# Kernel optimization log

Hardware: AMD Instinct MI355X
Metric: run time of the kernel (lower is better)

Reference implementation:

```python
import jax, jax.numpy as jnp
import numpy as np

N = 100000      # nodes
E = 800000      # edges (avg degree 8)
D_IN = 128      # in_channels
HEADS = 8
C = 16          # out_channels per head (heads*C = 128 output dim)
NEG_SLOPE = 0.2  # PyG GATConv default leaky_relu slope


def setup_inputs() -> dict:
    key = jax.random.key(0)
    ks = jax.random.split(key, 12)
    s = 1.0 / np.sqrt(D_IN)
    x = jax.random.normal(ks[0], (N, D_IN), jnp.float32)
    ei = jax.random.randint(ks[1], (2, E), 0, N, jnp.int32)
    return {
        "x": x,
        "ei": ei,
        # conv_in GATConv params
        "W_in": jax.random.normal(ks[2], (D_IN, HEADS * C), jnp.float32) * s,
        "a_src_in": jax.random.normal(ks[3], (HEADS, C), jnp.float32) * s,
        "a_dst_in": jax.random.normal(ks[4], (HEADS, C), jnp.float32) * s,
        "b_in": jnp.zeros((HEADS * C,), jnp.float32),
        # conv_out GATConv params (applied to flipped edges)
        "W_out": jax.random.normal(ks[5], (D_IN, HEADS * C), jnp.float32) * s,
        "a_src_out": jax.random.normal(ks[6], (HEADS, C), jnp.float32) * s,
        "a_dst_out": jax.random.normal(ks[7], (HEADS, C), jnp.float32) * s,
        "b_out": jnp.zeros((HEADS * C,), jnp.float32),
    }


def _gat_conv(x, src, dst, W, a_src, a_dst, b):
    # h: [N, H, C] projected node features
    h = (x @ W).reshape(N, HEADS, C)
    # per-node attention logits [N, H]
    alpha_src = jnp.einsum("nhc,hc->nh", h, a_src)
    alpha_dst = jnp.einsum("nhc,hc->nh", h, a_dst)
    # per-edge logits, message flows src -> dst; softmax grouped by dst
    logits = jax.nn.leaky_relu(alpha_src[src] + alpha_dst[dst], NEG_SLOPE)  # [E, H]
    seg_max = jax.ops.segment_max(logits, dst, num_segments=N)              # [N, H]
    ex = jnp.exp(logits - seg_max[dst])
    denom = jax.ops.segment_sum(ex, dst, num_segments=N)                    # [N, H]
    coef = ex / denom[dst]                                                  # [E, H]
    msg = h[src] * coef[:, :, None]                                         # [E, H, C]
    out = jax.ops.segment_sum(msg, dst, num_segments=N)                     # [N, H, C]
    return out.reshape(N, HEADS * C) + b


def reference(x, ei, W_in, a_src_in, a_dst_in, b_in, W_out, a_src_out, a_dst_out, b_out):
    src, dst = ei[0], ei[1]
    # DirSeq: conv_in on (src->dst), conv_out on flipped edges (dst->src)
    x_in = _gat_conv(x, src, dst, W_in, a_src_in, a_dst_in, b_in)
    x_out = _gat_conv(x, dst, src, W_out, a_src_out, a_dst_out, b_out)
    return x_in + x_out
```

## Files before the change

### kernel.cpp

```cpp
#include <hip/hip_runtime.h>

#define N_NODES 100000
#define N_EDGES 800000
#define NEG 0.2f
#define PB_SHIFT 8
#define PB_NODES 256
#define N_PBKT ((N_NODES + PB_NODES - 1) / PB_NODES)
#define TILE_E 4096
#define EPT 16
#define PREP_BLOCKS ((N_NODES * 128 / 4 + 255) / 256)
#define HIST_BLOCKS 192

typedef __attribute__((ext_vector_type(8))) short bf16x8;
typedef __attribute__((ext_vector_type(4))) float f32x4;

__device__ inline unsigned short f2bf(float f) {
    unsigned u = __float_as_uint(f);
    u += 0x7fffu + ((u >> 16) & 1u);
    return (unsigned short)(u >> 16);
}
__device__ inline float bf2f_lo(unsigned u) { return __uint_as_float(u << 16); }
__device__ inline float bf2f_hi(unsigned u) { return __uint_as_float(u & 0xffff0000u); }

__global__ __launch_bounds__(256) void prep_w_kernel(
    const float* __restrict__ W_in, const float* __restrict__ W_out,
    const float* __restrict__ as_in, const float* __restrict__ ad_in,
    const float* __restrict__ as_out, const float* __restrict__ ad_out,
    unsigned short* __restrict__ Wf, int* __restrict__ bcnt)
{
    const int t = blockIdx.x * 256 + threadIdx.x;
    if (t < 2 * N_PBKT) bcnt[t] = 0;
    if (t >= 2 * 4 * 9 * 64) return;
    const int lane = t & 63;
    const int rest = t >> 6;
    const int ct  = rest % 9;
    const int kb  = (rest / 9) & 3;
    const int dir = rest / 36;
    const float* W  = dir ? W_out  : W_in;
    const float* as = dir ? as_out : as_in;
    const float* ad = dir ? ad_out : ad_in;
    const int m16 = lane & 15, quad = lane >> 4;

    bf16x8 o;
#pragma unroll
    for (int j = 0; j < 8; ++j) {
        const int k = kb * 32 + quad * 8 + j;
        float v;
        if (ct < 8) {
            v = W[k * 128 + ct * 16 + m16];
        } else {
            const float* av = (m16 < 8) ? as : ad;
            const int hh = m16 & 7;
            v = 0.f;
            for (int c = 0; c < 16; ++c)
                v += W[k * 128 + hh * 16 + c] * av[hh * 16 + c];
        }
        o[j] = (short)f2bf(v);
    }
    *(bf16x8*)&Wf[(long long)t * 8] = o;
}

__global__ __launch_bounds__(256) void prep_hist_kernel(
    const float* __restrict__ x, unsigned short* __restrict__ x_bf,
    const int* __restrict__ ei, int* __restrict__ bcnt)
{
    const int tid = threadIdx.x;
    if (blockIdx.x < PREP_BLOCKS) {
        const int i = (blockIdx.x * 256 + tid) * 4;
        if (i >= N_NODES * 128) return;
        const float4 v = *(const float4*)&x[i];
        ushort4 o;
        o.x = f2bf(v.x); o.y = f2bf(v.y); o.z = f2bf(v.z); o.w = f2bf(v.w);
        *(ushort4*)&x_bf[i] = o;
        return;
    }
    __shared__ int bh[2 * N_PBKT];
    for (int i = tid; i < 2 * N_PBKT; i += 256) bh[i] = 0;
    __syncthreads();
    const int hb = blockIdx.x - PREP_BLOCKS;
    for (int e = hb * 256 + tid; e < N_EDGES; e += HIST_BLOCKS * 256) {
        const int s = ei[e];
        const int t = ei[N_EDGES + e];
        atomicAdd(&bh[t >> PB_SHIFT], 1);
        atomicAdd(&bh[N_PBKT + (s >> PB_SHIFT)], 1);
    }
    __syncthreads();
    for (int i = tid; i < 2 * N_PBKT; i += 256) {
        const int v = bh[i];
        if (v) atomicAdd(&bcnt[i], v);
    }
}

__global__ __launch_bounds__(256) void gemm_kernel(
    const unsigned short* __restrict__ x_bf,
    const unsigned short* __restrict__ Wf,
    unsigned short* __restrict__ h_in, unsigned short* __restrict__ h_out,
    float* __restrict__ asrc_in, float* __restrict__ adst_in,
    float* __restrict__ asrc_out, float* __restrict__ adst_out)
{
    const int dir = blockIdx.y;
    unsigned short* h = dir ? h_out : h_in;
    float* asrc = dir ? asrc_out : asrc_in;
    float* adst = dir ? adst_out : adst_in;

    const int tid  = threadIdx.x;
    const int lane = tid & 63;
    const int wave = tid >> 6;
    const int m16  = lane & 15;
    const int quad = lane >> 4;
    const int rbase = blockIdx.x * 128 + wave * 32;

    f32x4 acc[2][8];
    f32x4 acc_a[2];
#pragma unroll
    for (int rt = 0; rt < 2; ++rt) {
        acc_a[rt] = f32x4{0.f, 0.f, 0.f, 0.f};
#pragma unroll
        for (int ct = 0; ct < 8; ++ct)
            acc[rt][ct] = f32x4{0.f, 0.f, 0.f, 0.f};
    }

    const unsigned short* wf = Wf + (long long)dir * 4 * 9 * 64 * 8;

#pragma unroll
    for (int kb = 0; kb < 4; ++kb) {
        const int k0 = kb * 32 + quad * 8;
        bf16x8 a[2];
#pragma unroll
        for (int rt = 0; rt < 2; ++rt) {
            int r = rbase + rt * 16 + m16;
            r = r < N_NODES ? r : N_NODES - 1;
            a[rt] = *(const bf16x8*)&x_bf[(long long)r * 128 + k0];
        }
#pragma unroll
        for (int ct = 0; ct < 9; ++ct) {
            const bf16x8 b = *(const bf16x8*)&wf[(long long)((kb * 9 + ct) * 64 + lane) * 8];
            if (ct < 8) {
                acc[0][ct] = __builtin_amdgcn_mfma_f32_16x16x32_bf16(a[0], b, acc[0][ct], 0, 0, 0);
                acc[1][ct] = __builtin_amdgcn_mfma_f32_16x16x32_bf16(a[1], b, acc[1][ct], 0, 0, 0);
            } else {
                acc_a[0] = __builtin_amdgcn_mfma_f32_16x16x32_bf16(a[0], b, acc_a[0], 0, 0, 0);
                acc_a[1] = __builtin_amdgcn_mfma_f32_16x16x32_bf16(a[1], b, acc_a[1], 0, 0, 0);
            }
        }
    }

#pragma unroll
    for (int rt = 0; rt < 2; ++rt) {
#pragma unroll
        for (int r = 0; r < 4; ++r) {
            const int row = rbase + rt * 16 + quad * 4 + r;
            if (row < N_NODES) {
                unsigned short* hp = &h[(long long)row * 128 + m16];
#pragma unroll
                for (int ct = 0; ct < 8; ++ct)
                    hp[ct * 16] = f2bf(acc[rt][ct][r]);
                const float av = acc_a[rt][r];
                if (m16 < 8) asrc[row * 8 + m16] = av;
                else         adst[row * 8 + (m16 - 8)] = av;
            }
        }
    }
}

__global__ __launch_bounds__(512) void bucket_scan_kernel(
    const int* __restrict__ bcnt,
    int* __restrict__ boffs0, int* __restrict__ boffs1,
    int* __restrict__ gcur,
    int* __restrict__ offs_in, int* __restrict__ offs_out)
{
    const int dir = blockIdx.x;
    const int* c = bcnt + dir * N_PBKT;
    int* bo = dir ? boffs1 : boffs0;
    int* gc = gcur + dir * N_PBKT;

    __shared__ int sm[512];
    const int tid = threadIdx.x;
    const int v = (tid < N_PBKT) ? c[tid] : 0;
    sm[tid] = v;
    __syncthreads();
#pragma unroll
    for (int off = 1; off < 512; off <<= 1) {
        int t = (tid >= off) ? sm[tid - off] : 0;
        __syncthreads();
        sm[tid] += t;
        __syncthreads();
    }
    if (tid < N_PBKT) {
        const int excl = sm[tid] - v;
        bo[tid] = excl;
        gc[tid] = excl;
    }
    if (tid == N_PBKT - 1) bo[N_PBKT] = sm[tid];
    if (tid == 0) (dir ? offs_out : offs_in)[N_NODES] = N_EDGES;
}

__global__ __launch_bounds__(256) void partition_kernel(
    const int* __restrict__ ei, int* __restrict__ gcur,
    int* __restrict__ binned0, int* __restrict__ binned1)
{
    const int dir = blockIdx.y;
    int* binned = dir ? binned1 : binned0;
    int* gc = gcur + dir * N_PBKT;

    __shared__ int hist[N_PBKT];
    __shared__ int curs[N_PBKT];
    const int tid = threadIdx.x;
    for (int i = tid; i < N_PBKT; i += 256) hist[i] = 0;
    __syncthreads();

    const int e0 = blockIdx.x * TILE_E;
    int key[EPT], val[EPT];
#pragma unroll
    for (int i = 0; i < EPT; ++i) {
        const int e = e0 + i * 256 + tid;
        if (e < N_EDGES) {
            const int s = ei[e];
            const int t = ei[N_EDGES + e];
            key[i] = dir ? s : t;
            val[i] = dir ? t : s;
            atomicAdd(&hist[key[i] >> PB_SHIFT], 1);
        } else {
            key[i] = -1; val[i] = 0;
        }
    }
    __syncthreads();
    for (int b = tid; b < N_PBKT; b += 256) {
        const int c = hist[b];
        curs[b] = c ? atomicAdd(&gc[b], c) : 0;
    }
    __syncthreads();
#pragma unroll
    for (int i = 0; i < EPT; ++i) {
        if (key[i] >= 0) {
            const int pos = atomicAdd(&curs[key[i] >> PB_SHIFT], 1);
            binned[pos] = (val[i] << 8) | (key[i] & (PB_NODES - 1));
        }
    }
}

__global__ __launch_bounds__(256) void place_kernel(
    const int* __restrict__ binned0, const int* __restrict__ binned1,
    const int* __restrict__ boffs0, const int* __restrict__ boffs1,
    int* __restrict__ adj_in, int* __restrict__ adj_out,
    int* __restrict__ offs_in, int* __restrict__ offs_out)
{
    const int b   = blockIdx.x;
    const int dir = blockIdx.y;
    const int* bp = dir ? binned1 : binned0;
    const int* bo = dir ? boffs1  : boffs0;
    int* adj  = dir ? adj_out  : adj_in;
    int* offs = dir ? offs_out : offs_in;

    const int base = b << PB_SHIFT;
    const int beg = bo[b], end = bo[b + 1];
    const int tid = threadIdx.x;

    __shared__ int cnt[PB_NODES];
    __shared__ int sc[PB_NODES];
    __shared__ int cur[PB_NODES];

    cnt[tid] = 0;
    __syncthreads();
    for (int p = beg + tid; p < end; p += 256)
        atomicAdd(&cnt[bp[p] & (PB_NODES - 1)], 1);
    __syncthreads();
    const int v = cnt[tid];
    sc[tid] = v;
    __syncthreads();
#pragma unroll
    for (int off = 1; off < PB_NODES; off <<= 1) {
        int t = (tid >= off) ? sc[tid - off] : 0;
        __syncthreads();
        sc[tid] += t;
        __syncthreads();
    }
    const int excl = beg + sc[tid] - v;
    cur[tid] = excl;
    const int node = base + tid;
    if (node < N_NODES) offs[node] = excl;
    __syncthreads();
    for (int p = beg + tid; p < end; p += 256) {
        const int pk = bp[p];
        adj[atomicAdd(&cur[pk & (PB_NODES - 1)], 1)] = pk >> 8;
    }
}

__global__ __launch_bounds__(256) void gather_kernel(
    const int* __restrict__ offs_in, const int* __restrict__ adj_in,
    const int* __restrict__ offs_out, const int* __restrict__ adj_out,
    const unsigned short* __restrict__ h_in, const unsigned short* __restrict__ h_out,
    const float* __restrict__ asrc_in, const float* __restrict__ adst_in,
    const float* __restrict__ asrc_out, const float* __restrict__ adst_out,
    const float* __restrict__ b_in, const float* __restrict__ b_out,
    float* __restrict__ out)
{
    const int n = (blockIdx.x * 256 + threadIdx.x) >> 6;
    if (n >= N_NODES) return;
    const int lane = threadIdx.x & 63;
    const int c0 = lane * 2;
    const int hh = lane >> 3;
    const int g8 = lane & 7;
    const int grpbase = lane & 56;

    float acc0 = b_in[c0] + b_out[c0];
    float acc1 = b_in[c0 + 1] + b_out[c0 + 1];

#define DIR_BLOCK(OFFS, ADJ, HX, ASRC, ADST)                                   \
    {                                                                          \
        const int beg = OFFS[n], end = OFFS[n + 1];                            \
        if (end > beg) {                                                       \
            const float ad = ADST[n * 8 + hh];                                 \
            float num0 = 0.f, num1 = 0.f, den = 0.f;                           \
            int p = beg;                                                       \
            for (; p + 8 <= end; p += 8) {                                     \
                const int nb_mine = ADJ[p + g8];                               \
                float l = ASRC[nb_mine * 8 + hh] + ad;                         \
                l = l > 0.f ? l : NEG * l;                                     \
                const float w = __expf(l);                                     \
                den += w;                                                      \
                _Pragma("unroll")                                              \
                for (int g = 0; g < 8; ++g) {                                  \
                    const int   nb_g = __shfl(nb_mine, grpbase + g, 64);       \
                    const float w_g  = __shfl(w, grpbase + g, 64);             \
                    const unsigned hv = *(const unsigned*)&HX[(long long)nb_g * 128 + c0]; \
                    num0 += w_g * bf2f_lo(hv);                                 \
                    num1 += w_g * bf2f_hi(hv);                                 \
                }                                                              \
            }                                                                  \
            if (p < end) {                                                     \
                const int q = p + g8;                                          \
                const int nb_mine = (q < end) ? ADJ[q] : 0;                    \
                float w = 0.f;                                                 \
                if (q < end) {                                                 \
                    float l = ASRC[nb_mine * 8 + hh] + ad;                     \
                    l = l > 0.f ? l : NEG * l;                                 \
                    w = __expf(l);                                             \
                }                                                              \
                den += w;                                                      \
                const int cnt_t = end - p;                                     \
                for (int g = 0; g < cnt_t; ++g) {                              \
                    const int   nb_g = __shfl(nb_mine, grpbase + g, 64);       \
                    const float w_g  = __shfl(w, grpbase + g, 64);             \
                    const unsigned hv = *(const unsigned*)&HX[(long long)nb_g * 128 + c0]; \
                    num0 += w_g * bf2f_lo(hv);                                 \
                    num1 += w_g * bf2f_hi(hv);                                 \
                }                                                              \
            }                                                                  \
            den += __shfl_xor(den, 1, 64);                                     \
            den += __shfl_xor(den, 2, 64);                                     \
            den += __shfl_xor(den, 4, 64);                                     \
            acc0 += num0 / den;                                                \
            acc1 += num1 / den;                                                \
        }                                                                      \
    }

    DIR_BLOCK(offs_in, adj_in, h_in, asrc_in, adst_in)
    DIR_BLOCK(offs_out, adj_out, h_out, asrc_out, adst_out)
#undef DIR_BLOCK

    *(float2*)&out[(long long)n * 128 + c0] = float2{acc0, acc1};
}

extern "C" void kernel_launch(void* const* d_in, const int* in_sizes, int n_in,
                              void* d_out, int out_size, void* d_ws, size_t ws_size,
                              hipStream_t stream) {
    const float* x      = (const float*)d_in[0];
    const int*   ei     = (const int*)  d_in[1];
    const float* W_in   = (const float*)d_in[2];
    const float* as_in  = (const float*)d_in[3];
    const float* ad_in  = (const float*)d_in[4];
    const float* b_in   = (const float*)d_in[5];
    const float* W_out  = (const float*)d_in[6];
    const float* as_out = (const float*)d_in[7];
    const float* ad_out = (const float*)d_in[8];
    const float* b_out  = (const float*)d_in[9];
    float* out = (float*)d_out;

    char* ws = (char*)d_ws;
    const long long NH = (long long)N_NODES * 128;
    unsigned short* x_bf  = (unsigned short*)ws;    ws += NH * 2;
    unsigned short* h_in  = (unsigned short*)ws;    ws += NH * 2;
    unsigned short* h_out = (unsigned short*)ws;    ws += NH * 2;
    unsigned short* Wf    = (unsigned short*)ws;    ws += 2LL * 4 * 9 * 64 * 8 * 2;
    float* asrc_in   = (float*)ws;                  ws += N_NODES * 8 * 4;
    float* adst_in   = (float*)ws;                  ws += N_NODES * 8 * 4;
    float* asrc_out  = (float*)ws;                  ws += N_NODES * 8 * 4;
    float* adst_out  = (float*)ws;                  ws += N_NODES * 8 * 4;
    int* binned0     = (int*)ws;                    ws += (long long)N_EDGES * 4;
    int* binned1     = (int*)ws;                    ws += (long long)N_EDGES * 4;
    int* adj_in      = (int*)ws;                    ws += N_EDGES * 4;
    int* adj_out     = (int*)ws;                    ws += N_EDGES * 4;
    int* offs_in     = (int*)ws;                    ws += (N_NODES + 1) * 4;
    int* offs_out    = (int*)ws;                    ws += (N_NODES + 1) * 4;
    int* bcnt        = (int*)ws;                    ws += 2 * N_PBKT * 4;
    int* boffs0      = (int*)ws;                    ws += (N_PBKT + 1) * 4;
    int* boffs1      = (int*)ws;                    ws += (N_PBKT + 1) * 4;
    int* gcur        = (int*)ws;                    ws += 2 * N_PBKT * 4;

    prep_w_kernel<<<(2 * 4 * 9 * 64 + 255) / 256, 256, 0, stream>>>(
        W_in, W_out, as_in, ad_in, as_out, ad_out, Wf, bcnt);
    prep_hist_kernel<<<PREP_BLOCKS + HIST_BLOCKS, 256, 0, stream>>>(
        x, x_bf, ei, bcnt);

    dim3 gemm_grid((N_NODES + 127) / 128, 2);
    gemm_kernel<<<gemm_grid, 256, 0, stream>>>(
        x_bf, Wf, h_in, h_out, asrc_in, adst_in, asrc_out, adst_out);

    bucket_scan_kernel<<<2, 512, 0, stream>>>(
        bcnt, boffs0, boffs1, gcur, offs_in, offs_out);
    partition_kernel<<<dim3((N_EDGES + TILE_E - 1) / TILE_E, 2), 256, 0, stream>>>(
        ei, gcur, binned0, binned1);
    place_kernel<<<dim3(N_PBKT, 2), 256, 0, stream>>>(
        binned0, binned1, boffs0, boffs1, adj_in, adj_out, offs_in, offs_out);

    gather_kernel<<<(N_NODES * 64 + 255) / 256, 256, 0, stream>>>(
        offs_in, adj_in, offs_out, adj_out, h_in, h_out,
        asrc_in, adst_in, asrc_out, adst_out, b_in, b_out, out);
}
```

Baseline: 302.8 us.

## Precompute per-edge attention weights in place kernel, simplify gather loop

Moves the per-edge leaky-relu and exp computation from the gather kernel into the CSR placement kernel, which writes an edge-ordered [E,8] weight array alongside adj. The gather then reads precomputed weights and uniform (scalar) adjacency loads in a single loop with tail masking, using readfirstlane on the node index and a reciprocal instead of two divides. This removes random asrc gathers and exp work from the gather's critical path. In exchange it adds about 51 MB of extra weight writes and reads, plus padding writes for the masked tail.

```diff
diff --git a/kernel.cpp b/kernel.cpp
--- a/kernel.cpp
+++ b/kernel.cpp
@@ -21,15 +21,23 @@
 }
 __device__ inline float bf2f_lo(unsigned u) { return __uint_as_float(u << 16); }
 __device__ inline float bf2f_hi(unsigned u) { return __uint_as_float(u & 0xffff0000u); }
+__device__ inline float lexp(float l) { return __expf(l > 0.f ? l : NEG * l); }
 
 __global__ __launch_bounds__(256) void prep_w_kernel(
     const float* __restrict__ W_in, const float* __restrict__ W_out,
     const float* __restrict__ as_in, const float* __restrict__ ad_in,
     const float* __restrict__ as_out, const float* __restrict__ ad_out,
-    unsigned short* __restrict__ Wf, int* __restrict__ bcnt)
+    unsigned short* __restrict__ Wf, int* __restrict__ bcnt,
+    int* __restrict__ adj_in, int* __restrict__ adj_out,
+    float* __restrict__ w_in, float* __restrict__ w_out)
 {
     const int t = blockIdx.x * 256 + threadIdx.x;
     if (t < 2 * N_PBKT) bcnt[t] = 0;
+    if (t < 8) { adj_in[N_EDGES + t] = 0; adj_out[N_EDGES + t] = 0; }
+    if (t < 64) {
+        w_in[(long long)N_EDGES * 8 + t] = 0.f;
+        w_out[(long long)N_EDGES * 8 + t] = 0.f;
+    }
     if (t >= 2 * 4 * 9 * 64) return;
     const int lane = t & 63;
     const int rest = t >> 6;
@@ -243,7 +251,10 @@
     const int* __restrict__ binned0, const int* __restrict__ binned1,
     const int* __restrict__ boffs0, const int* __restrict__ boffs1,
     int* __restrict__ adj_in, int* __restrict__ adj_out,
-    int* __restrict__ offs_in, int* __restrict__ offs_out)
+    int* __restrict__ offs_in, int* __restrict__ offs_out,
+    const float* __restrict__ asrc_in, const float* __restrict__ adst_in,
+    const float* __restrict__ asrc_out, const float* __restrict__ adst_out,
+    float* __restrict__ w_in, float* __restrict__ w_out)
 {
     const int b   = blockIdx.x;
     const int dir = blockIdx.y;
@@ -251,6 +262,9 @@
     const int* bo = dir ? boffs1  : boffs0;
     int* adj  = dir ? adj_out  : adj_in;
     int* offs = dir ? offs_out : offs_in;
+    const float* asrc = dir ? asrc_out : asrc_in;
+    const float* adst = dir ? adst_out : adst_in;
+    float* wx = dir ? w_out : w_in;
 
     const int base = b << PB_SHIFT;
     const int beg = bo[b], end = bo[b + 1];
@@ -282,7 +296,21 @@
     __syncthreads();
     for (int p = beg + tid; p < end; p += 256) {
         const int pk = bp[p];
-        adj[atomicAdd(&cur[pk & (PB_NODES - 1)], 1)] = pk >> 8;
+        const int loc = pk & (PB_NODES - 1);
+        const int src = pk >> 8;
+        const int pos = atomicAdd(&cur[loc], 1);
+        adj[pos] = src;
+        const float4 s0 = *(const float4*)&asrc[src * 8];
+        const float4 s1 = *(const float4*)&asrc[src * 8 + 4];
+        const float4 d0 = *(const float4*)&adst[(base + loc) * 8];
+        const float4 d1 = *(const float4*)&adst[(base + loc) * 8 + 4];
+        float4 w0, w1;
+        w0.x = lexp(s0.x + d0.x); w0.y = lexp(s0.y + d0.y);
+        w0.z = lexp(s0.z + d0.z); w0.w = lexp(s0.w + d0.w);
+        w1.x = lexp(s1.x + d1.x); w1.y = lexp(s1.y + d1.y);
+        w1.z = lexp(s1.z + d1.z); w1.w = lexp(s1.w + d1.w);
+        *(float4*)&wx[(long long)pos * 8]     = w0;
+        *(float4*)&wx[(long long)pos * 8 + 4] = w1;
     }
 }
 
@@ -290,13 +318,13 @@
     const int* __restrict__ offs_in, const int* __restrict__ adj_in,
     const int* __restrict__ offs_out, const int* __restrict__ adj_out,
     const unsigned short* __restrict__ h_in, const unsigned short* __restrict__ h_out,
-    const float* __restrict__ asrc_in, const float* __restrict__ adst_in,
-    const float* __restrict__ asrc_out, const float* __restrict__ adst_out,
+    const float* __restrict__ w_in, const float* __restrict__ w_out,
     const float* __restrict__ b_in, const float* __restrict__ b_out,
     float* __restrict__ out)
 {
-    const int n = (blockIdx.x * 256 + threadIdx.x) >> 6;
+    int n = (blockIdx.x * 256 + threadIdx.x) >> 6;
     if (n >= N_NODES) return;
+    n = __builtin_amdgcn_readfirstlane(n);
     const int lane = threadIdx.x & 63;
     const int c0 = lane * 2;
     const int hh = lane >> 3;
@@ -306,43 +334,21 @@
     float acc0 = b_in[c0] + b_out[c0];
     float acc1 = b_in[c0 + 1] + b_out[c0 + 1];
 
-#define DIR_BLOCK(OFFS, ADJ, HX, ASRC, ADST)                                   \
+#define DIR_BLOCK(OFFS, ADJ, HX, WX)                                           \
     {                                                                          \
         const int beg = OFFS[n], end = OFFS[n + 1];                            \
         if (end > beg) {                                                       \
-            const float ad = ADST[n * 8 + hh];                                 \
             float num0 = 0.f, num1 = 0.f, den = 0.f;                           \
-            int p = beg;                                                       \
-            for (; p + 8 <= end; p += 8) {                                     \
-                const int nb_mine = ADJ[p + g8];                               \
-                float l = ASRC[nb_mine * 8 + hh] + ad;                         \
-                l = l > 0.f ? l : NEG * l;                                     \
-                const float w = __expf(l);                                     \
-                den += w;                                                      \
+            for (int p = beg; p < end; p += 8) {                               \
+                const int q = p + g8;                                          \
+                const float wl = (q < end) ? WX[(long long)q * 8 + hh] : 0.f;  \
+                den += wl;                                                     \
                 _Pragma("unroll")                                              \
                 for (int g = 0; g < 8; ++g) {                                  \
-                    const int   nb_g = __shfl(nb_mine, grpbase + g, 64);       \
-                    const float w_g  = __shfl(w, grpbase + g, 64);             \
-                    const unsigned hv = *(const unsigned*)&HX[(long long)nb_g * 128 + c0]; \
-                    num0 += w_g * bf2f_lo(hv);                                 \
-                    num1 += w_g * bf2f_hi(hv);                                 \
-                }                                                              \
-            }                                                                  \
-            if (p < end) {                                                     \
-                const int q = p + g8;                                          \
-                const int nb_mine = (q < end) ? ADJ[q] : 0;                    \
-                float w = 0.f;                                                 \
-                if (q < end) {                                                 \
-                    float l = ASRC[nb_mine * 8 + hh] + ad;                     \
-                    l = l > 0.f ? l : NEG * l;                                 \
-                    w = __expf(l);                                             \
-                }                                                              \
-                den += w;                                                      \
-                const int cnt_t = end - p;                                     \
-                for (int g = 0; g < cnt_t; ++g) {                              \
-                    const int   nb_g = __shfl(nb_mine, grpbase + g, 64);       \
-                    const float w_g  = __shfl(w, grpbase + g, 64);             \
-                    const unsigned hv = *(const unsigned*)&HX[(long long)nb_g * 128 + c0]; \
+                    const int qq = p + g;                                      \
+                    const int nb = (qq < end) ? ADJ[qq] : 0;       \
+                    const float w_g = __shfl(wl, grpbase + g, 64);             \
+                    const unsigned hv = *(const unsigned*)&HX[(long long)nb * 128 + c0]; \
                     num0 += w_g * bf2f_lo(hv);                                 \
                     num1 += w_g * bf2f_hi(hv);                                 \
                 }                                                              \
@@ -350,13 +356,14 @@
             den += __shfl_xor(den, 1, 64);                                     \
             den += __shfl_xor(den, 2, 64);                                     \
             den += __shfl_xor(den, 4, 64);                                     \
-            acc0 += num0 / den;                                                \
-            acc1 += num1 / den;                                                \
+            const float rden = 1.f / den;                                      \
+            acc0 += num0 * rden;                                               \
+            acc1 += num1 * rden;                                               \
         }                                                                      \
     }
 
-    DIR_BLOCK(offs_in, adj_in, h_in, asrc_in, adst_in)
-    DIR_BLOCK(offs_out, adj_out, h_out, asrc_out, adst_out)
+    DIR_BLOCK(offs_in, adj_in, h_in, w_in)
+    DIR_BLOCK(offs_out, adj_out, h_out, w_out)
 #undef DIR_BLOCK
 
     *(float2*)&out[(long long)n * 128 + c0] = float2{acc0, acc1};
@@ -387,10 +394,12 @@
     float* adst_in   = (float*)ws;                  ws += N_NODES * 8 * 4;
     float* asrc_out  = (float*)ws;                  ws += N_NODES * 8 * 4;
     float* adst_out  = (float*)ws;                  ws += N_NODES * 8 * 4;
+    float* w_arr_in  = (float*)ws;                  ws += ((long long)N_EDGES * 8 + 64) * 4;
+    float* w_arr_out = (float*)ws;                  ws += ((long long)N_EDGES * 8 + 64) * 4;
     int* binned0     = (int*)ws;                    ws += (long long)N_EDGES * 4;
     int* binned1     = (int*)ws;                    ws += (long long)N_EDGES * 4;
-    int* adj_in      = (int*)ws;                    ws += N_EDGES * 4;
-    int* adj_out     = (int*)ws;                    ws += N_EDGES * 4;
+    int* adj_in      = (int*)ws;                    ws += (N_EDGES + 8) * 4;
+    int* adj_out     = (int*)ws;                    ws += (N_EDGES + 8) * 4;
     int* offs_in     = (int*)ws;                    ws += (N_NODES + 1) * 4;
     int* offs_out    = (int*)ws;                    ws += (N_NODES + 1) * 4;
     int* bcnt        = (int*)ws;                    ws += 2 * N_PBKT * 4;
@@ -399,7 +408,8 @@
     int* gcur        = (int*)ws;                    ws += 2 * N_PBKT * 4;
 
     prep_w_kernel<<<(2 * 4 * 9 * 64 + 255) / 256, 256, 0, stream>>>(
-        W_in, W_out, as_in, ad_in, as_out, ad_out, Wf, bcnt);
+        W_in, W_out, as_in, ad_in, as_out, ad_out, Wf, bcnt,
+        adj_in, adj_out, w_arr_in, w_arr_out);
     prep_hist_kernel<<<PREP_BLOCKS + HIST_BLOCKS, 256, 0, stream>>>(
         x, x_bf, ei, bcnt);
 
@@ -412,9 +422,10 @@
     partition_kernel<<<dim3((N_EDGES + TILE_E - 1) / TILE_E, 2), 256, 0, stream>>>(
         ei, gcur, binned0, binned1);
     place_kernel<<<dim3(N_PBKT, 2), 256, 0, stream>>>(
-        binned0, binned1, boffs0, boffs1, adj_in, adj_out, offs_in, offs_out);
+        binned0, binned1, boffs0, boffs1, adj_in, adj_out, offs_in, offs_out,
+        asrc_in, adst_in, asrc_out, adst_out, w_arr_in, w_arr_out);
 
     gather_kernel<<<(N_NODES * 64 + 255) / 256, 256, 0, stream>>>(
         offs_in, adj_in, offs_out, adj_out, h_in, h_out,
-        asrc_in, adst_in, asrc_out, adst_out, b_in, b_out, out);
-}
+        w_arr_in, w_arr_out, b_in, b_out, out);
+}
```

Result: slower. 338.9 us (+11.9%).
